# Kernel optimization log

Measured on AMD Instinct MI355X. Metric: run time of the kernel, lower is better.

Reference implementation:

```python
import jax, jax.numpy as jnp
import numpy as np

TOP_K = 256
MAX_ITER = 25
EPS = 0.1  # Sinkhorn entropic regularization


def gmm_params(gamma, pts):
    # gamma: (B,K,J) soft assignments, pts: (B,K,D)
    pi = jnp.clip(gamma.mean(axis=1), 1e-4)                      # (B,J)
    Npi = pi * gamma.shape[1]                                     # (B,J)
    mu = jnp.einsum('bkj,bkd->bjd', gamma, pts) / Npi[..., None]  # (B,J,D)
    return pi, mu


def contrastsk(x, y, p, max_iter=MAX_ITER, eps=EPS):
    # x: (B,K,D) points, y: (B,J,D) centers, p: (B,J) column marginal (mixture weights)
    # squared euclidean cost (B,K,J)
    cost = (jnp.sum(x * x, -1)[:, :, None] + jnp.sum(y * y, -1)[:, None, :]
            - 2.0 * jnp.einsum('bkd,bjd->bkj', x, y))
    log_K = -cost / eps
    B, K, J = log_K.shape
    log_r = jnp.full((B, K), -jnp.log(jnp.float32(K)))            # uniform rows
    log_c = jnp.log(jnp.clip(p / jnp.sum(p, -1, keepdims=True), 1e-9))

    def body(carry, _):
        log_u, log_v = carry
        log_u = log_r - jax.nn.logsumexp(log_K + log_v[:, None, :], axis=2)
        log_v = log_c - jax.nn.logsumexp(log_K + log_u[:, :, None], axis=1)
        return (log_u, log_v), None

    init = (jnp.zeros((B, K), cost.dtype), jnp.zeros((B, J), cost.dtype))
    (log_u, log_v), _ = jax.lax.scan(body, init, None, length=max_iter)
    T = jnp.exp(log_u[:, :, None] + log_K + log_v[:, None, :])    # transport plan (B,K,J)
    dis = jnp.sum(T * cost)
    return T, dis


def reference(pts, log_gamma, prob):
    # top-k most confident points
    topk_ids = jax.lax.top_k(prob, TOP_K)[1]                      # (B,topk)
    log_score = jnp.take_along_axis(log_gamma, topk_ids[..., None], axis=1)  # (B,topk,J)
    pts_g = jnp.take_along_axis(pts, topk_ids[..., None], axis=1)            # (B,topk,D)
    score = jax.nn.softmax(log_score, axis=-1)
    pi, mu = gmm_params(score, pts_g)
    assign, _dis = contrastsk(pts_g, mu, pi)
    assign = assign / jnp.clip(assign.sum(-1, keepdims=True), 1e-4)
    assign = jax.lax.stop_gradient(assign)                        # torch.no_grad + detach
    loss = jnp.mean(jnp.sum(-assign * jax.nn.log_softmax(log_score, axis=-1), axis=1))
    return loss


def setup_inputs() -> dict:
    key = jax.random.key(0)
    k1, k2, k3 = jax.random.split(key, 3)
    B, N, J, D = 128, 4096, 256, 3
    return {
        'pts': jax.random.normal(k1, (B, N, D), jnp.float32),
        'log_gamma': jax.random.normal(k2, (B, N, J), jnp.float32),
        'prob': jax.random.uniform(k3, (B, N), jnp.float32),
    }
```

## Files before the change

### kernel.cpp

```cpp
#include <hip/hip_runtime.h>
#include <stdint.h>

#define NB 128
#define NN 4096
#define NJ 256
#define NK 256
#define NITER 25

__device__ __forceinline__ float wredf(float v) {
#pragma unroll
  for (int o = 32; o > 0; o >>= 1) v += __shfl_xor(v, o, 64);
  return v;
}

__global__ __launch_bounds__(256) void km_main(
    const float* __restrict__ pts, const float* __restrict__ lg,
    const float* __restrict__ prob, float* __restrict__ kw,
    float* __restrict__ bloss) {
  const int b = blockIdx.x;
  const int t = threadIdx.x;
  const int lane = t & 63, wid = t >> 6;

  __shared__ unsigned long long keys[NN];
  __shared__ int hist[4096];
  __shared__ int warr[4];
  __shared__ int ifind[2];
  __shared__ int cnt_sh;
  __shared__ int idxl[NK];
  __shared__ __align__(16) float x4[NK * 4];
  __shared__ __align__(16) float mu4[NJ * 4];
  __shared__ float ckv[NK];
  __shared__ float cjv[NJ];
  __shared__ float av[NK];
  __shared__ __align__(16) float bv[NJ];
  __shared__ float redf4[4];

  const float* pb = prob + (size_t)b * NN;
  for (int i = t; i < NN; i += 256) {
    unsigned bits = __float_as_uint(pb[i]);
    keys[i] = ((unsigned long long)bits << 12) | (unsigned)(4095 - i);
  }
  unsigned long long theta = 0ull;
  int need = NK;
  const int shv[4] = {32, 20, 8, 0};
  const int psv[4] = {44, 32, 20, 8};
  __syncthreads();
#pragma unroll 1
  for (int L = 0; L < 4; ++L) {
    const int sh = shv[L], ps = psv[L];
    for (int i = t; i < 4096; i += 256) hist[i] = 0;
    __syncthreads();
    for (int i = t; i < NN; i += 256) {
      unsigned long long kk = keys[i];
      if ((kk >> ps) == (theta >> ps))
        atomicAdd(&hist[(int)((kk >> sh) & 0xFFFull)], 1);
    }
    __syncthreads();
    int loc[16];
    int tot = 0;
#pragma unroll
    for (int q = 15; q >= 0; --q) { loc[q] = tot; tot += hist[16 * t + q]; }
    int s = tot;
#pragma unroll
    for (int o = 1; o < 64; o <<= 1) {
      int u = __shfl_down(s, o, 64);
      if (lane + o < 64) s += u;
    }
    if (lane == 0) warr[wid] = s;
    __syncthreads();
    int gtw = s - tot;
    for (int w = wid + 1; w < 4; ++w) gtw += warr[w];
#pragma unroll
    for (int q = 0; q < 16; ++q) {
      int g = gtw + loc[q];
      int h = hist[16 * t + q];
      if (g < need && g + h >= need) { ifind[0] = 16 * t + q; ifind[1] = g; }
    }
    __syncthreads();
    theta |= ((unsigned long long)ifind[0]) << sh;
    need -= ifind[1];
    __syncthreads();
  }
  if (t == 0) cnt_sh = 0;
  __syncthreads();
  for (int i = t; i < NN; i += 256) {
    if (keys[i] >= theta) {
      int p = atomicAdd(&cnt_sh, 1);
      idxl[p] = 4095 - (int)(keys[i] & 0xFFFull);
    }
  }
  __syncthreads();

  const int myi = idxl[t];
  const float* xr = pts + ((size_t)b * NN + myi) * 3;
  const float px = xr[0], py = xr[1], pz = xr[2];
  x4[4 * t] = px; x4[4 * t + 1] = py; x4[4 * t + 2] = pz; x4[4 * t + 3] = 0.f;
  const float* lr = lg + ((size_t)b * NN + myi) * NJ;
  float m = -3.4e38f;
#pragma unroll 4
  for (int j = 0; j < NJ; j += 4) {
    float4 v = *(const float4*)(lr + j);
    m = fmaxf(m, fmaxf(fmaxf(v.x, v.y), fmaxf(v.z, v.w)));
  }
  float zz = 0.f;
#pragma unroll 4
  for (int j = 0; j < NJ; j += 4) {
    float4 v = *(const float4*)(lr + j);
    zz += __expf(v.x - m) + __expf(v.y - m) + __expf(v.z - m) + __expf(v.w - m);
  }
  const float myck = m + __logf(zz);
  ckv[t] = myck;
  __syncthreads();

  {
    const float* lgb = lg + (size_t)b * NN * NJ;
    float pi = 0.f, a0 = 0.f, a1 = 0.f, a2 = 0.f;
#pragma unroll 4
    for (int k = 0; k < NK; ++k) {
      float lv = lgb[(size_t)idxl[k] * NJ + t];
      float S = __expf(lv - ckv[k]);
      float4 xx = *(const float4*)&x4[4 * k];
      pi += S;
      a0 = fmaf(S, xx.x, a0); a1 = fmaf(S, xx.y, a1); a2 = fmaf(S, xx.z, a2);
    }
    float pim = fmaxf(pi * (1.f / 256.f), 1e-4f);
    float npi = pim * 256.f;
    float m0 = a0 / npi, m1 = a1 / npi, m2 = a2 / npi;
    mu4[4 * t] = m0; mu4[4 * t + 1] = m1; mu4[4 * t + 2] = m2;
    mu4[4 * t + 3] = -14.426950408889634f * (m0 * m0 + m1 * m1 + m2 * m2);
    float ssum = wredf(pim);
    if (lane == 0) redf4[wid] = ssum;
    __syncthreads();
    float tot = redf4[0] + redf4[1] + redf4[2] + redf4[3];
    cjv[t] = fmaxf(pim / tot, 1e-9f);
  }
  __syncthreads();

  {
    const float xp0 = px * 28.853900817779268f;
    const float xp1 = py * 28.853900817779268f;
    const float xp2 = pz * 28.853900817779268f;
    float rm = -3.4e38f;
#pragma unroll 4
    for (int j = 0; j < NJ; ++j) {
      float4 mm = *(const float4*)&mu4[4 * j];
      float sj = fmaf(xp0, mm.x, fmaf(xp1, mm.y, fmaf(xp2, mm.z, mm.w)));
      rm = fmaxf(rm, sj);
    }
    float* krow = kw + (((size_t)b << 16) + ((size_t)t << 8));
#pragma unroll 2
    for (int j = 0; j < NJ; j += 4) {
      float4 mm0 = *(const float4*)&mu4[4 * j];
      float4 mm1 = *(const float4*)&mu4[4 * (j + 1)];
      float4 mm2 = *(const float4*)&mu4[4 * (j + 2)];
      float4 mm3 = *(const float4*)&mu4[4 * (j + 3)];
      float4 o;
      o.x = exp2f(fmaf(xp0, mm0.x, fmaf(xp1, mm0.y, fmaf(xp2, mm0.z, mm0.w))) - rm);
      o.y = exp2f(fmaf(xp0, mm1.x, fmaf(xp1, mm1.y, fmaf(xp2, mm1.z, mm1.w))) - rm);
      o.z = exp2f(fmaf(xp0, mm2.x, fmaf(xp1, mm2.y, fmaf(xp2, mm2.z, mm2.w))) - rm);
      o.w = exp2f(fmaf(xp0, mm3.x, fmaf(xp1, mm3.y, fmaf(xp2, mm3.z, mm3.w))) - rm);
      *(float4*)(krow + j) = o;
    }
    bv[t] = 1.f;
  }
  __syncthreads();

  const float* kbase = kw + ((size_t)b << 16);
  const float4* kr4 = (const float4*)(kbase + ((size_t)t << 8));
  const float4* bv4 = (const float4*)bv;
#pragma unroll 1
  for (int it = 0; it < NITER; ++it) {
    float acc = 0.f;
#pragma unroll 8
    for (int j4 = 0; j4 < 64; ++j4) {
      float4 kv = kr4[j4];
      float4 b4 = bv4[j4];
      acc = fmaf(kv.x, b4.x, fmaf(kv.y, b4.y, fmaf(kv.z, b4.z, fmaf(kv.w, b4.w, acc))));
    }
    av[t] = (1.f / 256.f) / fmaxf(acc, 1e-35f);
    __syncthreads();
    float acc2 = 0.f;
    const float* kc = kbase + t;
#pragma unroll 16
    for (int k = 0; k < NK; ++k) acc2 = fmaf(kc[(size_t)k << 8], av[k], acc2);
    bv[t] = cjv[t] / fmaxf(acc2, 1e-35f);
    __syncthreads();
  }

  {
    float rs = 0.f;
#pragma unroll 8
    for (int j4 = 0; j4 < 64; ++j4) {
      float4 kv = kr4[j4];
      float4 b4 = bv4[j4];
      rs = fmaf(kv.x, b4.x, fmaf(kv.y, b4.y, fmaf(kv.z, b4.z, fmaf(kv.w, b4.w, rs))));
    }
    const float atk = av[t];
    const float fko = atk / fmaxf(atk * rs, 1e-4f);
    const float* lr2 = lg + ((size_t)b * NN + myi) * NJ;
    float acc = 0.f;
#pragma unroll 4
    for (int j4 = 0; j4 < 64; ++j4) {
      float4 kv = kr4[j4];
      float4 b4 = bv4[j4];
      float4 l4 = *(const float4*)(lr2 + 4 * j4);
      acc = fmaf(kv.x * b4.x, myck - l4.x, acc);
      acc = fmaf(kv.y * b4.y, myck - l4.y, acc);
      acc = fmaf(kv.z * b4.z, myck - l4.z, acc);
      acc = fmaf(kv.w * b4.w, myck - l4.w, acc);
    }
    float lk = fko * acc;
    float s2 = wredf(lk);
    if (lane == 0) redf4[wid] = s2;
    __syncthreads();
    if (t == 0) bloss[b] = redf4[0] + redf4[1] + redf4[2] + redf4[3];
  }
}

__global__ __launch_bounds__(128) void km_fin(const float* __restrict__ bloss,
                                              float* __restrict__ out) {
  int t = threadIdx.x;
  float v = bloss[t];
  v = wredf(v);
  __shared__ float r2[2];
  if ((t & 63) == 0) r2[t >> 6] = v;
  __syncthreads();
  if (t == 0) out[0] = (r2[0] + r2[1]) * (1.f / 32768.f);
}

extern "C" void kernel_launch(void* const* d_in, const int* in_sizes, int n_in,
                              void* d_out, int out_size, void* d_ws, size_t ws_size,
                              hipStream_t stream) {
  const float* pts = (const float*)d_in[0];
  const float* lg = (const float*)d_in[1];
  const float* prob = (const float*)d_in[2];
  float* kw = (float*)d_ws;
  float* bloss = (float*)((char*)d_ws + (size_t)NB * 65536 * 4);
  km_main<<<NB, 256, 0, stream>>>(pts, lg, prob, kw, bloss);
  km_fin<<<1, 128, 0, stream>>>(bloss, (float*)d_out);
}
```

Baseline: 980.1 us.

## Use 1024 threads per batch with quad-split rows and register-resident kernel matrix

```diff
diff --git a/kernel.cpp b/kernel.cpp
--- a/kernel.cpp
+++ b/kernel.cpp
@@ -6,214 +6,261 @@
 #define NJ 256
 #define NK 256
 #define NITER 25
+#define PAD 68
 
 __device__ __forceinline__ float wredf(float v) {
 #pragma unroll
   for (int o = 32; o > 0; o >>= 1) v += __shfl_xor(v, o, 64);
   return v;
 }
-
-__global__ __launch_bounds__(256) void km_main(
+__device__ __forceinline__ float qsum(float v) {
+  v += __shfl_xor(v, 1, 64);
+  v += __shfl_xor(v, 2, 64);
+  return v;
+}
+__device__ __forceinline__ float qmax(float v) {
+  v = fmaxf(v, __shfl_xor(v, 1, 64));
+  v = fmaxf(v, __shfl_xor(v, 2, 64));
+  return v;
+}
+
+__global__ __launch_bounds__(1024) void km_main(
     const float* __restrict__ pts, const float* __restrict__ lg,
     const float* __restrict__ prob, float* __restrict__ kw,
     float* __restrict__ bloss) {
   const int b = blockIdx.x;
   const int t = threadIdx.x;
-  const int lane = t & 63, wid = t >> 6;
-
-  __shared__ unsigned long long keys[NN];
-  __shared__ int hist[4096];
-  __shared__ int warr[4];
+  const int lane = t & 63, w = t >> 6;
+  const int kj = t >> 2, q = t & 3;
+
+  __shared__ __align__(16) int pool[4096];
+  __shared__ int warr[16];
+  __shared__ float warf[16];
   __shared__ int ifind[2];
   __shared__ int cnt_sh;
-  __shared__ int idxl[NK];
-  __shared__ __align__(16) float x4[NK * 4];
-  __shared__ __align__(16) float mu4[NJ * 4];
-  __shared__ float ckv[NK];
-  __shared__ float cjv[NJ];
-  __shared__ float av[NK];
-  __shared__ __align__(16) float bv[NJ];
-  __shared__ float redf4[4];
+
+  int* hist = pool;
+  int(*idxp)[PAD] = (int(*)[PAD])pool;
+  float(*ckvp)[PAD] = (float(*)[PAD])((char*)pool + 1088);
+  float(*avp)[PAD] = (float(*)[PAD])((char*)pool + 2176);
+  float(*bvp)[PAD] = (float(*)[PAD])((char*)pool + 3264);
+  float4(*x4p)[65] = (float4(*)[65])((char*)pool + 4352);
+  float4(*mup)[65] = (float4(*)[65])((char*)pool + 8512);
+  float(*fgp)[136] = (float(*)[136])((char*)pool + 12672);
+  float* cjv = (float*)((char*)pool + 14848);
 
   const float* pb = prob + (size_t)b * NN;
-  for (int i = t; i < NN; i += 256) {
-    unsigned bits = __float_as_uint(pb[i]);
-    keys[i] = ((unsigned long long)bits << 12) | (unsigned)(4095 - i);
-  }
+  unsigned pbits[4];
+#pragma unroll
+  for (int r = 0; r < 4; ++r) pbits[r] = __float_as_uint(pb[t + 1024 * r]);
+
   unsigned long long theta = 0ull;
   int need = NK;
   const int shv[4] = {32, 20, 8, 0};
   const int psv[4] = {44, 32, 20, 8};
-  __syncthreads();
 #pragma unroll 1
   for (int L = 0; L < 4; ++L) {
     const int sh = shv[L], ps = psv[L];
-    for (int i = t; i < 4096; i += 256) hist[i] = 0;
-    __syncthreads();
-    for (int i = t; i < NN; i += 256) {
-      unsigned long long kk = keys[i];
+    for (int i = t; i < 4096; i += 1024) hist[i] = 0;
+    __syncthreads();
+#pragma unroll
+    for (int r = 0; r < 4; ++r) {
+      int i = t + 1024 * r;
+      unsigned long long kk =
+          ((unsigned long long)pbits[r] << 12) | (unsigned)(4095 - i);
       if ((kk >> ps) == (theta >> ps))
         atomicAdd(&hist[(int)((kk >> sh) & 0xFFFull)], 1);
     }
     __syncthreads();
-    int loc[16];
+    int loc[4];
     int tot = 0;
 #pragma unroll
-    for (int q = 15; q >= 0; --q) { loc[q] = tot; tot += hist[16 * t + q]; }
+    for (int qq = 3; qq >= 0; --qq) { loc[qq] = tot; tot += hist[4 * t + qq]; }
     int s = tot;
 #pragma unroll
     for (int o = 1; o < 64; o <<= 1) {
       int u = __shfl_down(s, o, 64);
       if (lane + o < 64) s += u;
     }
-    if (lane == 0) warr[wid] = s;
+    if (lane == 0) warr[w] = s;
     __syncthreads();
     int gtw = s - tot;
-    for (int w = wid + 1; w < 4; ++w) gtw += warr[w];
-#pragma unroll
-    for (int q = 0; q < 16; ++q) {
-      int g = gtw + loc[q];
-      int h = hist[16 * t + q];
-      if (g < need && g + h >= need) { ifind[0] = 16 * t + q; ifind[1] = g; }
+    for (int w2 = w + 1; w2 < 16; ++w2) gtw += warr[w2];
+#pragma unroll
+    for (int qq = 0; qq < 4; ++qq) {
+      int g = gtw + loc[qq];
+      int h = hist[4 * t + qq];
+      if (g < need && g + h >= need) { ifind[0] = 4 * t + qq; ifind[1] = g; }
     }
     __syncthreads();
     theta |= ((unsigned long long)ifind[0]) << sh;
     need -= ifind[1];
-    __syncthreads();
   }
   if (t == 0) cnt_sh = 0;
   __syncthreads();
-  for (int i = t; i < NN; i += 256) {
-    if (keys[i] >= theta) {
+#pragma unroll
+  for (int r = 0; r < 4; ++r) {
+    int i = t + 1024 * r;
+    unsigned long long kk =
+        ((unsigned long long)pbits[r] << 12) | (unsigned)(4095 - i);
+    if (kk >= theta) {
       int p = atomicAdd(&cnt_sh, 1);
-      idxl[p] = 4095 - (int)(keys[i] & 0xFFFull);
-    }
-  }
-  __syncthreads();
-
-  const int myi = idxl[t];
+      idxp[p >> 6][p & 63] = i;
+    }
+  }
+  __syncthreads();
+
+  const int myi = idxp[kj >> 6][kj & 63];
   const float* xr = pts + ((size_t)b * NN + myi) * 3;
   const float px = xr[0], py = xr[1], pz = xr[2];
-  x4[4 * t] = px; x4[4 * t + 1] = py; x4[4 * t + 2] = pz; x4[4 * t + 3] = 0.f;
-  const float* lr = lg + ((size_t)b * NN + myi) * NJ;
-  float m = -3.4e38f;
-#pragma unroll 4
-  for (int j = 0; j < NJ; j += 4) {
-    float4 v = *(const float4*)(lr + j);
-    m = fmaxf(m, fmaxf(fmaxf(v.x, v.y), fmaxf(v.z, v.w)));
-  }
+  if (q == 0) x4p[kj >> 6][kj & 63] = make_float4(px, py, pz, 0.f);
+  const float4* lr4 = (const float4*)(lg + ((size_t)b * NN + myi) * NJ + q * 64);
+  float lvv[64];
+  float rmB = -3.4e38f;
+#pragma unroll
+  for (int m4 = 0; m4 < 16; ++m4) {
+    float4 v = lr4[m4];
+    lvv[4 * m4] = v.x; lvv[4 * m4 + 1] = v.y;
+    lvv[4 * m4 + 2] = v.z; lvv[4 * m4 + 3] = v.w;
+    rmB = fmaxf(rmB, fmaxf(fmaxf(v.x, v.y), fmaxf(v.z, v.w)));
+  }
+  rmB = qmax(rmB);
   float zz = 0.f;
-#pragma unroll 4
-  for (int j = 0; j < NJ; j += 4) {
-    float4 v = *(const float4*)(lr + j);
-    zz += __expf(v.x - m) + __expf(v.y - m) + __expf(v.z - m) + __expf(v.w - m);
-  }
-  const float myck = m + __logf(zz);
-  ckv[t] = myck;
-  __syncthreads();
-
+#pragma unroll
+  for (int m = 0; m < 64; ++m) zz += __expf(lvv[m] - rmB);
+  zz = qsum(zz);
+  const float myck = rmB + __logf(zz);
+  if (q == 0) ckvp[kj >> 6][kj & 63] = myck;
+  __syncthreads();
+
+  const float* lgb = lg + (size_t)b * NN * NJ;
   {
-    const float* lgb = lg + (size_t)b * NN * NJ;
     float pi = 0.f, a0 = 0.f, a1 = 0.f, a2 = 0.f;
-#pragma unroll 4
-    for (int k = 0; k < NK; ++k) {
-      float lv = lgb[(size_t)idxl[k] * NJ + t];
-      float S = __expf(lv - ckv[k]);
-      float4 xx = *(const float4*)&x4[4 * k];
+#pragma unroll 8
+    for (int n = 0; n < 64; ++n) {
+      int kk2 = idxp[q][n];
+      float lv = lgb[(size_t)kk2 * NJ + kj];
+      float S = __expf(lv - ckvp[q][n]);
+      float4 xx = x4p[q][n];
       pi += S;
       a0 = fmaf(S, xx.x, a0); a1 = fmaf(S, xx.y, a1); a2 = fmaf(S, xx.z, a2);
     }
+    pi = qsum(pi); a0 = qsum(a0); a1 = qsum(a1); a2 = qsum(a2);
     float pim = fmaxf(pi * (1.f / 256.f), 1e-4f);
     float npi = pim * 256.f;
     float m0 = a0 / npi, m1 = a1 / npi, m2 = a2 / npi;
-    mu4[4 * t] = m0; mu4[4 * t + 1] = m1; mu4[4 * t + 2] = m2;
-    mu4[4 * t + 3] = -14.426950408889634f * (m0 * m0 + m1 * m1 + m2 * m2);
-    float ssum = wredf(pim);
-    if (lane == 0) redf4[wid] = ssum;
-    __syncthreads();
-    float tot = redf4[0] + redf4[1] + redf4[2] + redf4[3];
-    cjv[t] = fmaxf(pim / tot, 1e-9f);
-  }
-  __syncthreads();
-
+    if (q == 0)
+      mup[kj >> 6][kj & 63] = make_float4(
+          m0, m1, m2, -14.426950408889634f * (m0 * m0 + m1 * m1 + m2 * m2));
+    float cc = (q == 0) ? pim : 0.f;
+    cc = wredf(cc);
+    if (lane == 0) warf[w] = cc;
+    __syncthreads();
+    float totp = 0.f;
+#pragma unroll
+    for (int i = 0; i < 16; ++i) totp += warf[i];
+    if (q == 0) cjv[kj] = fmaxf(pim / totp, 1e-9f);
+  }
+
+  float kreg[64];
   {
     const float xp0 = px * 28.853900817779268f;
     const float xp1 = py * 28.853900817779268f;
     const float xp2 = pz * 28.853900817779268f;
     float rm = -3.4e38f;
-#pragma unroll 4
-    for (int j = 0; j < NJ; ++j) {
-      float4 mm = *(const float4*)&mu4[4 * j];
-      float sj = fmaf(xp0, mm.x, fmaf(xp1, mm.y, fmaf(xp2, mm.z, mm.w)));
-      rm = fmaxf(rm, sj);
-    }
-    float* krow = kw + (((size_t)b << 16) + ((size_t)t << 8));
-#pragma unroll 2
-    for (int j = 0; j < NJ; j += 4) {
-      float4 mm0 = *(const float4*)&mu4[4 * j];
-      float4 mm1 = *(const float4*)&mu4[4 * (j + 1)];
-      float4 mm2 = *(const float4*)&mu4[4 * (j + 2)];
-      float4 mm3 = *(const float4*)&mu4[4 * (j + 3)];
-      float4 o;
-      o.x = exp2f(fmaf(xp0, mm0.x, fmaf(xp1, mm0.y, fmaf(xp2, mm0.z, mm0.w))) - rm);
-      o.y = exp2f(fmaf(xp0, mm1.x, fmaf(xp1, mm1.y, fmaf(xp2, mm1.z, mm1.w))) - rm);
-      o.z = exp2f(fmaf(xp0, mm2.x, fmaf(xp1, mm2.y, fmaf(xp2, mm2.z, mm2.w))) - rm);
-      o.w = exp2f(fmaf(xp0, mm3.x, fmaf(xp1, mm3.y, fmaf(xp2, mm3.z, mm3.w))) - rm);
-      *(float4*)(krow + j) = o;
-    }
-    bv[t] = 1.f;
-  }
-  __syncthreads();
-
-  const float* kbase = kw + ((size_t)b << 16);
-  const float4* kr4 = (const float4*)(kbase + ((size_t)t << 8));
-  const float4* bv4 = (const float4*)bv;
+#pragma unroll
+    for (int m = 0; m < 64; ++m) {
+      float4 mm = mup[q][m];
+      float sv = fmaf(xp0, mm.x, fmaf(xp1, mm.y, fmaf(xp2, mm.z, mm.w)));
+      kreg[m] = sv;
+      rm = fmaxf(rm, sv);
+    }
+    rm = qmax(rm);
+#pragma unroll
+    for (int m = 0; m < 64; ++m) kreg[m] = exp2f(kreg[m] - rm);
+    float4* kst4 = (float4*)(kw + ((size_t)b << 16) + (size_t)kj * 256 + q * 64);
+#pragma unroll
+    for (int m4 = 0; m4 < 16; ++m4)
+      kst4[m4] = make_float4(kreg[4 * m4], kreg[4 * m4 + 1], kreg[4 * m4 + 2],
+                             kreg[4 * m4 + 3]);
+    if (t < 256) bvp[t >> 6][t & 63] = 1.f;
+  }
+  __syncthreads();
+
+  const float* kcb = kw + ((size_t)b << 16) + (size_t)(q * 64) * 256 + kj;
+  const float4* bq4 = (const float4*)(&bvp[q][0]);
+  const float4* aq4 = (const float4*)(&avp[q][0]);
+  float aval = 0.f;
 #pragma unroll 1
   for (int it = 0; it < NITER; ++it) {
-    float acc = 0.f;
+    float r0 = 0.f, r1 = 0.f, r2 = 0.f, r3 = 0.f;
+#pragma unroll
+    for (int m4 = 0; m4 < 16; ++m4) {
+      float4 bb = bq4[m4];
+      r0 = fmaf(kreg[4 * m4], bb.x, r0);
+      r1 = fmaf(kreg[4 * m4 + 1], bb.y, r1);
+      r2 = fmaf(kreg[4 * m4 + 2], bb.z, r2);
+      r3 = fmaf(kreg[4 * m4 + 3], bb.w, r3);
+    }
+    float acc = qsum((r0 + r1) + (r2 + r3));
+    aval = (1.f / 256.f) / fmaxf(acc, 1e-35f);
+    if (q == 0) avp[kj >> 6][kj & 63] = aval;
+    __syncthreads();
+    float c0 = 0.f, c1 = 0.f;
 #pragma unroll 8
-    for (int j4 = 0; j4 < 64; ++j4) {
-      float4 kv = kr4[j4];
-      float4 b4 = bv4[j4];
-      acc = fmaf(kv.x, b4.x, fmaf(kv.y, b4.y, fmaf(kv.z, b4.z, fmaf(kv.w, b4.w, acc))));
-    }
-    av[t] = (1.f / 256.f) / fmaxf(acc, 1e-35f);
-    __syncthreads();
-    float acc2 = 0.f;
-    const float* kc = kbase + t;
-#pragma unroll 16
-    for (int k = 0; k < NK; ++k) acc2 = fmaf(kc[(size_t)k << 8], av[k], acc2);
-    bv[t] = cjv[t] / fmaxf(acc2, 1e-35f);
+    for (int n4 = 0; n4 < 16; ++n4) {
+      float4 a4 = aq4[n4];
+      c0 = fmaf(kcb[(size_t)(4 * n4) * 256], a4.x, c0);
+      c1 = fmaf(kcb[(size_t)(4 * n4 + 1) * 256], a4.y, c1);
+      c0 = fmaf(kcb[(size_t)(4 * n4 + 2) * 256], a4.z, c0);
+      c1 = fmaf(kcb[(size_t)(4 * n4 + 3) * 256], a4.w, c1);
+    }
+    float acc2 = qsum(c0 + c1);
+    float bnew = cjv[kj] / fmaxf(acc2, 1e-35f);
+    if (q == 0) bvp[kj >> 6][kj & 63] = bnew;
     __syncthreads();
   }
 
   {
-    float rs = 0.f;
-#pragma unroll 8
-    for (int j4 = 0; j4 < 64; ++j4) {
-      float4 kv = kr4[j4];
-      float4 b4 = bv4[j4];
-      rs = fmaf(kv.x, b4.x, fmaf(kv.y, b4.y, fmaf(kv.z, b4.z, fmaf(kv.w, b4.w, rs))));
-    }
-    const float atk = av[t];
-    const float fko = atk / fmaxf(atk * rs, 1e-4f);
-    const float* lr2 = lg + ((size_t)b * NN + myi) * NJ;
-    float acc = 0.f;
+    float r0 = 0.f, r1 = 0.f, r2 = 0.f, r3 = 0.f;
+#pragma unroll
+    for (int m4 = 0; m4 < 16; ++m4) {
+      float4 bb = bq4[m4];
+      r0 = fmaf(kreg[4 * m4], bb.x, r0);
+      r1 = fmaf(kreg[4 * m4 + 1], bb.y, r1);
+      r2 = fmaf(kreg[4 * m4 + 2], bb.z, r2);
+      r3 = fmaf(kreg[4 * m4 + 3], bb.w, r3);
+    }
+    float rs = qsum((r0 + r1) + (r2 + r3));
+    float fko = aval / fmaxf(aval * rs, 1e-4f);
+    if (q == 0) {
+      fgp[kj >> 6][2 * (kj & 63)] = fko;
+      fgp[kj >> 6][2 * (kj & 63) + 1] = fko * myck;
+    }
+    __syncthreads();
+    float bj = bvp[kj >> 6][kj & 63];
+    const float2* fg2 = (const float2*)(&fgp[q][0]);
+    float la = 0.f, lb2 = 0.f;
 #pragma unroll 4
-    for (int j4 = 0; j4 < 64; ++j4) {
-      float4 kv = kr4[j4];
-      float4 b4 = bv4[j4];
-      float4 l4 = *(const float4*)(lr2 + 4 * j4);
-      acc = fmaf(kv.x * b4.x, myck - l4.x, acc);
-      acc = fmaf(kv.y * b4.y, myck - l4.y, acc);
-      acc = fmaf(kv.z * b4.z, myck - l4.z, acc);
-      acc = fmaf(kv.w * b4.w, myck - l4.w, acc);
-    }
-    float lk = fko * acc;
-    float s2 = wredf(lk);
-    if (lane == 0) redf4[wid] = s2;
-    __syncthreads();
-    if (t == 0) bloss[b] = redf4[0] + redf4[1] + redf4[2] + redf4[3];
+    for (int n = 0; n < 64; ++n) {
+      float Kv = kcb[(size_t)n * 256];
+      int kk2 = idxp[q][n];
+      float lgv = lgb[(size_t)kk2 * NJ + kj];
+      float2 fg = fg2[n];
+      la = fmaf(Kv, fg.y, la);
+      lb2 = fmaf(Kv * fg.x, lgv, lb2);
+    }
+    float accF = qsum(la - lb2);
+    float v = (q == 0) ? bj * accF : 0.f;
+    v = wredf(v);
+    if (lane == 0) warf[w] = v;
+    __syncthreads();
+    if (t == 0) {
+      float sv = 0.f;
+#pragma unroll
+      for (int i = 0; i < 16; ++i) sv += warf[i];
+      bloss[b] = sv;
+    }
   }
 }
 
@@ -236,6 +283,6 @@
   const float* prob = (const float*)d_in[2];
   float* kw = (float*)d_ws;
   float* bloss = (float*)((char*)d_ws + (size_t)NB * 65536 * 4);
-  km_main<<<NB, 256, 0, stream>>>(pts, lg, prob, kw, bloss);
+  km_main<<<NB, 1024, 0, stream>>>(pts, lg, prob, kw, bloss);
   km_fin<<<1, 128, 0, stream>>>(bloss, (float*)d_out);
 }
```

Result: faster. 841.1 us (-14.2%).
